# Optimization experiments

Measured on AMD Instinct MI355X. Metric: run time of the kernel, lower is better.

## Reference

```python
import jax, jax.numpy as jnp
import numpy as np

STRIDE = 1
PADDING = 1


def _ternarize(w):
    # threshold = 0.75 * mean(|w|); alpha = mean(|w| over |w| > threshold)
    abs_w = jnp.abs(w)
    threshold = 0.75 * jnp.mean(abs_w)
    mask = abs_w > threshold
    cnt = jnp.sum(mask)
    alpha = jnp.where(cnt > 0, jnp.sum(jnp.where(mask, abs_w, 0.0)) / jnp.maximum(cnt, 1), 1.0)
    tern = jnp.where(w > threshold, alpha, jnp.where(w < -threshold, -alpha, 0.0))
    # straight-through estimator: forward uses tern, grad flows to w as identity
    return w + jax.lax.stop_gradient(tern - w)


def setup_inputs() -> dict:
    key = jax.random.key(0)
    k_x, k_w = jax.random.split(key)
    x = jax.random.normal(k_x, (32, 256, 56, 56), dtype=jnp.float32)
    weight = jax.random.normal(k_w, (256, 256, 3, 3), dtype=jnp.float32)
    return {"x": x, "weight": weight}


def reference(x, weight):
    tw = _ternarize(weight)
    # NCHW input, OIHW kernel
    return jax.lax.conv_general_dilated(
        x, tw,
        window_strides=(STRIDE, STRIDE),
        padding=[(PADDING, PADDING), (PADDING, PADDING)],
        dimension_numbers=("NCHW", "OIHW", "NCHW"),
    )
```

## Files before the change

### kernel.cpp

```cpp
#include <hip/hip_runtime.h>
#include <hip/hip_bf16.h>

typedef short short8 __attribute__((ext_vector_type(8)));
typedef float f32x4 __attribute__((ext_vector_type(4)));

constexpr int N_  = 32;
constexpr int C_  = 256;
constexpr int K_  = 256;
constexpr int H_  = 56;
constexpr int W_  = 56;
constexpr int HW_ = H_ * W_;
constexpr int NW_ = K_ * C_ * 9;

constexpr int TH   = 4;
constexpr int NB   = 14;
constexpr int HR   = 6, HC = 58;
constexpr int NH   = HR * HC;
constexpr int BROW = 80;
constexpr int BSZ  = NH * BROW;
constexpr int NPAIR2 = 8 * NH;
constexpr int SITER  = 6;
constexpr int ASTEP  = 16384;

constexpr int NQB   = 1152;
constexpr int WS_P1 = 4;
constexpr int WS_P2 = 300;
constexpr int WS_P3 = 1500;
constexpr size_t WS_WQ = 16384;
constexpr size_t WS_NEEDED = WS_WQ + (size_t)NW_ * 2;

__device__ __forceinline__ unsigned f2bf(float f) {
    unsigned u = __builtin_bit_cast(unsigned, f);
    return (u + 0x7FFFu + ((u >> 16) & 1u)) >> 16;
}

__global__ void k_abs_partial(const float* __restrict__ w, float* __restrict__ ws) {
    __shared__ float sm[4];
    float s = 0.f;
    for (int i = blockIdx.x * 256 + threadIdx.x; i < NW_; i += 256 * 256)
        s += fabsf(w[i]);
    #pragma unroll
    for (int o = 32; o > 0; o >>= 1) s += __shfl_down(s, o, 64);
    const int wid = threadIdx.x >> 6, lane = threadIdx.x & 63;
    if (lane == 0) sm[wid] = s;
    __syncthreads();
    if (threadIdx.x == 0) {
        float r = 0.f;
        for (int i = 0; i < 4; ++i) r += sm[i];
        ws[WS_P1 + blockIdx.x] = r;
    }
}

__device__ __forceinline__ float reduce256_all(const float* __restrict__ p, float* sm) {
    float v = threadIdx.x < 256 ? p[threadIdx.x] : 0.f;
    #pragma unroll
    for (int o = 32; o > 0; o >>= 1) v += __shfl_down(v, o, 64);
    const int wid = threadIdx.x >> 6, lane = threadIdx.x & 63;
    __syncthreads();
    if (lane == 0) sm[wid] = v;
    __syncthreads();
    float total = 0.f;
    #pragma unroll
    for (int i = 0; i < 8; ++i) total += sm[i];
    return total;
}

__global__ __launch_bounds__(512) void k_quant(const float* __restrict__ w,
                                               float* __restrict__ ws,
                                               unsigned short* __restrict__ wq) {
    __shared__ float sm[8];
    const float total = reduce256_all(ws + WS_P1, sm);
    const float thr = 0.75f * total / (float)NW_;
    const int i = blockIdx.x * 512 + threadIdx.x;
    const float v = w[i];
    const unsigned short q = v > thr ? (unsigned short)0x3F80
                                     : (v < -thr ? (unsigned short)0xBF80 : (unsigned short)0);
    const int k   = i / 2304;
    const int rem = i - k * 2304;
    const int c   = rem / 9;
    const int rs  = rem - c * 9;
    const int chi = c >> 5, c5 = c & 31;
    wq[(size_t)(chi * 9 + rs) * 8192 + (k << 5) + c5] = q;
    const float a = fabsf(v);
    float s = a > thr ? a : 0.f;
    float cn = a > thr ? 1.f : 0.f;
    #pragma unroll
    for (int o = 32; o > 0; o >>= 1) { s += __shfl_down(s, o, 64); cn += __shfl_down(cn, o, 64); }
    __shared__ float sm2[16];
    const int wid = threadIdx.x >> 6, lane = threadIdx.x & 63;
    __syncthreads();
    if (lane == 0) { sm2[wid] = s; sm2[8 + wid] = cn; }
    __syncthreads();
    if (threadIdx.x == 0) {
        float S = 0.f, C2 = 0.f;
        for (int j = 0; j < 8; ++j) { S += sm2[j]; C2 += sm2[8 + j]; }
        ws[WS_P2 + blockIdx.x] = S;
        ws[WS_P3 + blockIdx.x] = C2;
    }
}

__global__ void k_fb_total(float* __restrict__ ws) {
    __shared__ float sm[4];
    float v = ws[WS_P1 + threadIdx.x];
    #pragma unroll
    for (int o = 32; o > 0; o >>= 1) v += __shfl_down(v, o, 64);
    const int wid = threadIdx.x >> 6, lane = threadIdx.x & 63;
    if (lane == 0) sm[wid] = v;
    __syncthreads();
    if (threadIdx.x == 0) {
        float r = 0.f;
        for (int i = 0; i < 4; ++i) r += sm[i];
        ws[0] = r;
    }
}

__global__ void k_fb_masked(const float* __restrict__ w, float* __restrict__ ws) {
    const float thr = 0.75f * ws[0] / (float)NW_;
    float s = 0.f, c = 0.f;
    for (int i = blockIdx.x * 256 + threadIdx.x; i < NW_; i += 256 * 256) {
        float a = fabsf(w[i]);
        if (a > thr) { s += a; c += 1.f; }
    }
    #pragma unroll
    for (int o = 32; o > 0; o >>= 1) { s += __shfl_down(s, o, 64); c += __shfl_down(c, o, 64); }
    __shared__ float sm[8];
    const int wid = threadIdx.x >> 6, lane = threadIdx.x & 63;
    if (lane == 0) { sm[wid] = s; sm[4 + wid] = c; }
    __syncthreads();
    if (threadIdx.x == 0) {
        float S = 0.f, C2 = 0.f;
        for (int i = 0; i < 4; ++i) { S += sm[i]; C2 += sm[i + 4]; }
        ws[WS_P2 + blockIdx.x] = S;
        ws[WS_P3 + blockIdx.x] = C2;
    }
}

__global__ void k_final_masked(float* __restrict__ ws) {
    __shared__ float sm[8];
    float s = ws[WS_P2 + threadIdx.x];
    float c = ws[WS_P3 + threadIdx.x];
    #pragma unroll
    for (int o = 32; o > 0; o >>= 1) { s += __shfl_down(s, o, 64); c += __shfl_down(c, o, 64); }
    const int wid = threadIdx.x >> 6, lane = threadIdx.x & 63;
    if (lane == 0) { sm[wid] = s; sm[4 + wid] = c; }
    __syncthreads();
    if (threadIdx.x == 0) {
        float S = 0.f, C2 = 0.f;
        for (int i = 0; i < 4; ++i) { S += sm[i]; C2 += sm[i + 4]; }
        ws[1] = S; ws[2] = C2;
    }
}

constexpr int RSO_[9] = {
    (0*HC+0)*BROW, (0*HC+1)*BROW, (0*HC+2)*BROW,
    (1*HC+0)*BROW, (1*HC+1)*BROW, (1*HC+2)*BROW,
    (2*HC+0)*BROW, (2*HC+1)*BROW, (2*HC+2)*BROW };

struct ConvState {
    const float* xn;
    const char*  wqc;
    char*        ldsp;
    size_t       aoff;
    int          h0, tid;
    int          bB[7];
};

__device__ __forceinline__ void load_a(short8 (&d)[4], const ConvState& st, int step) {
    const char* ap = st.wqc + (size_t)step * ASTEP + st.aoff;
    d[0] = *(const short8*)(ap);
    d[1] = *(const short8*)(ap + 1024);
    d[2] = *(const short8*)(ap + 2048);
    d[3] = *(const short8*)(ap + 3072);
}

__device__ __forceinline__ void issue_b(const ConvState& st, int c0,
                                        float (&bs)[SITER][4], unsigned& bmask) {
    bmask = 0;
    #pragma unroll
    for (int it = 0; it < SITER; ++it) {
        const int u  = it * 512 + st.tid;
        const bool vu = u < NPAIR2;
        const int uu = vu ? u : 0;
        const int c4 = uu / NH, hidx = uu - c4 * NH;
        const int hy = hidx / HC, hx = hidx - hy * HC;
        const int h  = st.h0 - 1 + hy, w = hx - 1;
        const bool ok = vu && (unsigned)h < (unsigned)H_ && (unsigned)w < (unsigned)W_;
        const int off = ok ? ((c0 + 4 * c4) * HW_ + h * W_ + w) : 0;
        const float* p = st.xn + off;
        bs[it][0] = p[0];
        bs[it][1] = p[HW_];
        bs[it][2] = p[2 * HW_];
        bs[it][3] = p[3 * HW_];
        bmask |= (ok ? 1u : 0u) << it;
    }
}

__device__ __forceinline__ void write_b(const ConvState& st, int base,
                                        const float (&bs)[SITER][4], unsigned bmask) {
    #pragma unroll
    for (int it = 0; it < SITER; ++it) {
        const int u = it * 512 + st.tid;
        if (u < NPAIR2) {
            const int c4 = u / NH, hidx = u - c4 * NH;
            const bool ok = (bmask >> it) & 1u;
            const float f0 = ok ? bs[it][0] : 0.f;
            const float f1 = ok ? bs[it][1] : 0.f;
            const float f2 = ok ? bs[it][2] : 0.f;
            const float f3 = ok ? bs[it][3] : 0.f;
            uint2 v;
            v.x = f2bf(f0) | (f2bf(f1) << 16);
            v.y = f2bf(f2) | (f2bf(f3) << 16);
            *(uint2*)(st.ldsp + base + hidx * BROW + c4 * 8) = v;
        }
    }
}

template <int PAR, bool LASTCH>
__device__ __forceinline__ void do_chunk(int chi, const ConvState& st,
                                         short8 (&afr)[2][4], f32x4 (&acc)[4][7],
                                         float (&bs)[SITER][4], unsigned& bmask) {
    const int rdbase = PAR * BSZ;
    #pragma unroll
    for (int rs = 0; rs < 9; ++rs) {
        const int cur = (PAR + rs) & 1, nxt = cur ^ 1;
        const int step = chi * 9 + rs;
        if (!(LASTCH && rs == 8))
            load_a(afr[nxt], st, step + 1);

        short8 bfr[7];
        #pragma unroll
        for (int nf = 0; nf < 7; ++nf)
            bfr[nf] = *(const short8*)(st.ldsp + rdbase + st.bB[nf] + RSO_[rs]);

        __builtin_amdgcn_s_setprio(1);
        #pragma unroll
        for (int nf = 0; nf < 7; ++nf)
            #pragma unroll
            for (int mf = 0; mf < 4; ++mf)
                acc[mf][nf] = __builtin_amdgcn_mfma_f32_16x16x32_bf16(
                    afr[cur][mf], bfr[nf], acc[mf][nf], 0, 0, 0);
        __builtin_amdgcn_s_setprio(0);

        if (rs == 6 && !LASTCH)
            issue_b(st, (chi + 1) * 32, bs, bmask);
        if (rs == 8 && !LASTCH) {
            write_b(st, (PAR ^ 1) * BSZ, bs, bmask);
            asm volatile("s_waitcnt lgkmcnt(0)" ::: "memory");
            __builtin_amdgcn_s_barrier();
        }
    }
}

__global__ __launch_bounds__(512, 2) void conv_mfma(const float* __restrict__ x,
                                                    const unsigned short* __restrict__ wq,
                                                    const float* __restrict__ wsc,
                                                    float* __restrict__ out) {
    __shared__ char lds[2 * BSZ];
    const int tid = threadIdx.x, lane = tid & 63, wid = tid >> 6;
    const int wm = wid & 3, wn = wid >> 2, lr = lane & 15, lg = lane >> 4;
    const int band = blockIdx.x, n = blockIdx.y;

    ConvState st;
    st.xn   = x + (size_t)n * C_ * HW_;
    st.wqc  = (const char*)wq;
    st.ldsp = lds;
    st.aoff = (size_t)(wm * 64 + lr) * 64 + lg * 16;
    st.h0   = band * TH;
    st.tid  = tid;
    #pragma unroll
    for (int nf = 0; nf < 7; ++nf) {
        const int pos = wn * 112 + nf * 16 + lr;
        const int y = pos / 56, xx = pos - y * 56;
        st.bB[nf] = (y * HC + xx) * BROW + lg * 16;
    }

    f32x4 acc[4][7] = {};
    short8 afr[2][4];
    float bs[SITER][4];
    unsigned bmask;

    issue_b(st, 0, bs, bmask);
    load_a(afr[0], st, 0);
    write_b(st, 0, bs, bmask);
    asm volatile("s_waitcnt lgkmcnt(0)" ::: "memory");
    __builtin_amdgcn_s_barrier();

    for (int cc = 0; cc < 3; ++cc) {
        do_chunk<0, false>(2 * cc,     st, afr, acc, bs, bmask);
        do_chunk<1, false>(2 * cc + 1, st, afr, acc, bs, bmask);
    }
    do_chunk<0, false>(6, st, afr, acc, bs, bmask);
    do_chunk<1, true >(7, st, afr, acc, bs, bmask);

    __syncthreads();
    float* sred = (float*)lds;
    float s2 = wsc[WS_P2 + tid] + wsc[WS_P2 + 512 + tid];
    float s3 = wsc[WS_P3 + tid] + wsc[WS_P3 + 512 + tid];
    if (tid < NQB - 1024) {
        s2 += wsc[WS_P2 + 1024 + tid];
        s3 += wsc[WS_P3 + 1024 + tid];
    }
    #pragma unroll
    for (int o = 32; o > 0; o >>= 1) { s2 += __shfl_down(s2, o, 64); s3 += __shfl_down(s3, o, 64); }
    if (lane == 0) { sred[wid] = s2; sred[8 + wid] = s3; }
    __syncthreads();
    float msum = 0.f, mcnt = 0.f;
    #pragma unroll
    for (int i = 0; i < 8; ++i) { msum += sred[i]; mcnt += sred[8 + i]; }
    const float alpha = mcnt > 0.f ? msum / fmaxf(mcnt, 1.f) : 1.0f;

    #pragma unroll
    for (int mf = 0; mf < 4; ++mf) {
        const int k = wm * 64 + mf * 16 + lg * 4;
        #pragma unroll
        for (int nf = 0; nf < 7; ++nf) {
            const int pos = wn * 112 + nf * 16 + lr;
            const int y = pos / 56, xx = pos - y * 56;
            float* po = out + ((size_t)n * K_ + k) * HW_ + (st.h0 + y) * W_ + xx;
            #pragma unroll
            for (int j = 0; j < 4; ++j)
                po[(size_t)j * HW_] = alpha * acc[mf][nf][j];
        }
    }
}

constexpr int W4_ = W_ / 4;
constexpr int SP_ = H_ * W4_;
__global__ __launch_bounds__(256) void conv_tern_otf(const float* __restrict__ x,
                                                     const float* __restrict__ wt,
                                                     const float* __restrict__ wsc,
                                                     float* __restrict__ out) {
    const int kg = blockIdx.x, n = blockIdx.y, k0 = kg * 4;
    const float thr = 0.75f * wsc[0] / (float)NW_;
    const float cnt = wsc[2];
    const float alpha = cnt > 0.f ? wsc[1] / fmaxf(cnt, 1.f) : 1.0f;
    for (int j = 0; j < 4; ++j) {
        const int sp = (int)threadIdx.x + j * 256;
        if (sp >= SP_) break;
        const int h = sp / W4_, w0 = (sp % W4_) * 4;
        float acc[4][4];
        #pragma unroll
        for (int kt = 0; kt < 4; ++kt)
            #pragma unroll
            for (int jj = 0; jj < 4; ++jj) acc[kt][jj] = 0.f;
        for (int c = 0; c < C_; ++c) {
            const float* xp = x + (((size_t)n * C_ + c) * H_) * W_;
            float xr[3][6];
            #pragma unroll
            for (int r = 0; r < 3; ++r) {
                const int hh = h + r - 1;
                const float* rowp = xp + hh * W_;
                if ((unsigned)hh < (unsigned)H_) {
                    const float4 mid = *(const float4*)(rowp + w0);
                    xr[r][1] = mid.x; xr[r][2] = mid.y; xr[r][3] = mid.z; xr[r][4] = mid.w;
                    xr[r][0] = (w0 > 0)      ? rowp[w0 - 1] : 0.f;
                    xr[r][5] = (w0 + 4 < W_) ? rowp[w0 + 4] : 0.f;
                } else {
                    #pragma unroll
                    for (int q = 0; q < 6; ++q) xr[r][q] = 0.f;
                }
            }
            #pragma unroll
            for (int kt = 0; kt < 4; ++kt) {
                const float* wp = wt + ((size_t)(k0 + kt) * C_ + c) * 9;
                #pragma unroll
                for (int r = 0; r < 3; ++r)
                    #pragma unroll
                    for (int s = 0; s < 3; ++s) {
                        float wv = wp[r * 3 + s];
                        wv = wv > thr ? alpha : (wv < -thr ? -alpha : 0.f);
                        #pragma unroll
                        for (int jj = 0; jj < 4; ++jj)
                            acc[kt][jj] = fmaf(wv, xr[r][jj + s], acc[kt][jj]);
                    }
            }
        }
        #pragma unroll
        for (int kt = 0; kt < 4; ++kt) {
            float4 o;
            o.x = acc[kt][0]; o.y = acc[kt][1]; o.z = acc[kt][2]; o.w = acc[kt][3];
            *(float4*)(out + ((((size_t)n * K_ + (k0 + kt)) * H_ + h) * W_ + w0)) = o;
        }
    }
}

extern "C" void kernel_launch(void* const* d_in, const int* in_sizes, int n_in,
                              void* d_out, int out_size, void* d_ws, size_t ws_size,
                              hipStream_t stream) {
    const float* x = (const float*)d_in[0];
    const float* w = (const float*)d_in[1];
    float* out = (float*)d_out;
    float* ws  = (float*)d_ws;
    unsigned short* wq = (unsigned short*)((char*)d_ws + WS_WQ);

    k_abs_partial<<<256, 256, 0, stream>>>(w, ws);

    if (ws_size >= WS_NEEDED) {
        k_quant<<<NQB, 512, 0, stream>>>(w, ws, wq);
        dim3 grid(NB, N_);
        conv_mfma<<<grid, 512, 0, stream>>>(x, wq, ws, out);
    } else {
        k_fb_total<<<1, 256, 0, stream>>>(ws);
        k_fb_masked<<<256, 256, 0, stream>>>(w, ws);
        k_final_masked<<<1, 256, 0, stream>>>(ws);
        dim3 grid(64, N_);
        conv_tern_otf<<<grid, 256, 0, stream>>>(x, w, ws, out);
    }
}
```

Before: 128.3 us.

## Split output channels across two 256-thread blocks and stage B loads in two phases

The conv kernel now uses 256-thread blocks with four waves, and each block covers half of the 256 output channels, selected by a new kz index. The grid doubles along x so that twice as many blocks exist. Loading the input tile into LDS is split into two staged issue/write phases (6 then 5 iterations) spread across the filter taps, which bounds register use. Each block still stages the full input halo, so global and LDS input traffic and the bf16 conversion work are duplicated per output-channel half, in exchange for smaller blocks and more of them per CU.

```diff
diff --git a/kernel.cpp b/kernel.cpp
--- a/kernel.cpp
+++ b/kernel.cpp
@@ -19,7 +19,6 @@
 constexpr int BROW = 80;
 constexpr int BSZ  = NH * BROW;
 constexpr int NPAIR2 = 8 * NH;
-constexpr int SITER  = 6;
 constexpr int ASTEP  = 16384;
 
 constexpr int NQB   = 1152;
@@ -173,12 +172,13 @@
     d[3] = *(const short8*)(ap + 3072);
 }
 
-__device__ __forceinline__ void issue_b(const ConvState& st, int c0,
-                                        float (&bs)[SITER][4], unsigned& bmask) {
+template <int IT0, int NIT>
+__device__ __forceinline__ void issue_bx(const ConvState& st, int c0,
+                                         float (&bs)[6][4], unsigned& bmask) {
     bmask = 0;
     #pragma unroll
-    for (int it = 0; it < SITER; ++it) {
-        const int u  = it * 512 + st.tid;
+    for (int j = 0; j < NIT; ++j) {
+        const int u  = (IT0 + j) * 256 + st.tid;
         const bool vu = u < NPAIR2;
         const int uu = vu ? u : 0;
         const int c4 = uu / NH, hidx = uu - c4 * NH;
@@ -187,26 +187,27 @@
         const bool ok = vu && (unsigned)h < (unsigned)H_ && (unsigned)w < (unsigned)W_;
         const int off = ok ? ((c0 + 4 * c4) * HW_ + h * W_ + w) : 0;
         const float* p = st.xn + off;
-        bs[it][0] = p[0];
-        bs[it][1] = p[HW_];
-        bs[it][2] = p[2 * HW_];
-        bs[it][3] = p[3 * HW_];
-        bmask |= (ok ? 1u : 0u) << it;
-    }
-}
-
-__device__ __forceinline__ void write_b(const ConvState& st, int base,
-                                        const float (&bs)[SITER][4], unsigned bmask) {
-    #pragma unroll
-    for (int it = 0; it < SITER; ++it) {
-        const int u = it * 512 + st.tid;
+        bs[j][0] = p[0];
+        bs[j][1] = p[HW_];
+        bs[j][2] = p[2 * HW_];
+        bs[j][3] = p[3 * HW_];
+        bmask |= (ok ? 1u : 0u) << j;
+    }
+}
+
+template <int IT0, int NIT>
+__device__ __forceinline__ void write_bx(const ConvState& st, int base,
+                                         const float (&bs)[6][4], unsigned bmask) {
+    #pragma unroll
+    for (int j = 0; j < NIT; ++j) {
+        const int u = (IT0 + j) * 256 + st.tid;
         if (u < NPAIR2) {
             const int c4 = u / NH, hidx = u - c4 * NH;
-            const bool ok = (bmask >> it) & 1u;
-            const float f0 = ok ? bs[it][0] : 0.f;
-            const float f1 = ok ? bs[it][1] : 0.f;
-            const float f2 = ok ? bs[it][2] : 0.f;
-            const float f3 = ok ? bs[it][3] : 0.f;
+            const bool ok = (bmask >> j) & 1u;
+            const float f0 = ok ? bs[j][0] : 0.f;
+            const float f1 = ok ? bs[j][1] : 0.f;
+            const float f2 = ok ? bs[j][2] : 0.f;
+            const float f3 = ok ? bs[j][3] : 0.f;
             uint2 v;
             v.x = f2bf(f0) | (f2bf(f1) << 16);
             v.y = f2bf(f2) | (f2bf(f3) << 16);
@@ -218,8 +219,9 @@
 template <int PAR, bool LASTCH>
 __device__ __forceinline__ void do_chunk(int chi, const ConvState& st,
                                          short8 (&afr)[2][4], f32x4 (&acc)[4][7],
-                                         float (&bs)[SITER][4], unsigned& bmask) {
+                                         float (&bs)[6][4], unsigned& bmask) {
     const int rdbase = PAR * BSZ;
+    const int wrbase = (PAR ^ 1) * BSZ;
     #pragma unroll
     for (int rs = 0; rs < 9; ++rs) {
         const int cur = (PAR + rs) & 1, nxt = cur ^ 1;
@@ -241,30 +243,35 @@
                     afr[cur][mf], bfr[nf], acc[mf][nf], 0, 0, 0);
         __builtin_amdgcn_s_setprio(0);
 
-        if (rs == 6 && !LASTCH)
-            issue_b(st, (chi + 1) * 32, bs, bmask);
-        if (rs == 8 && !LASTCH) {
-            write_b(st, (PAR ^ 1) * BSZ, bs, bmask);
-            asm volatile("s_waitcnt lgkmcnt(0)" ::: "memory");
-            __builtin_amdgcn_s_barrier();
+        if (!LASTCH) {
+            if (rs == 4) {
+                issue_bx<0, 6>(st, (chi + 1) * 32, bs, bmask);
+            } else if (rs == 6) {
+                write_bx<0, 6>(st, wrbase, bs, bmask);
+                issue_bx<6, 5>(st, (chi + 1) * 32, bs, bmask);
+            } else if (rs == 8) {
+                write_bx<6, 5>(st, wrbase, bs, bmask);
+                asm volatile("s_waitcnt lgkmcnt(0)" ::: "memory");
+                __builtin_amdgcn_s_barrier();
+            }
         }
     }
 }
 
-__global__ __launch_bounds__(512, 2) void conv_mfma(const float* __restrict__ x,
+__global__ __launch_bounds__(256, 2) void conv_mfma(const float* __restrict__ x,
                                                     const unsigned short* __restrict__ wq,
                                                     const float* __restrict__ wsc,
                                                     float* __restrict__ out) {
     __shared__ char lds[2 * BSZ];
     const int tid = threadIdx.x, lane = tid & 63, wid = tid >> 6;
-    const int wm = wid & 3, wn = wid >> 2, lr = lane & 15, lg = lane >> 4;
-    const int band = blockIdx.x, n = blockIdx.y;
-
+    const int wm = wid & 1, wn = wid >> 1, lr = lane & 15, lg = lane >> 4;
+    const int bx = blockIdx.x, n = blockIdx.y;
+    const int band = bx >> 1, kz = bx & 1;
     ConvState st;
     st.xn   = x + (size_t)n * C_ * HW_;
     st.wqc  = (const char*)wq;
     st.ldsp = lds;
-    st.aoff = (size_t)(wm * 64 + lr) * 64 + lg * 16;
+    st.aoff = (size_t)(kz * 128 + wm * 64 + lr) * 64 + lg * 16;
     st.h0   = band * TH;
     st.tid  = tid;
     #pragma unroll
@@ -276,12 +283,14 @@
 
     f32x4 acc[4][7] = {};
     short8 afr[2][4];
-    float bs[SITER][4];
+    float bs[6][4];
     unsigned bmask;
 
-    issue_b(st, 0, bs, bmask);
     load_a(afr[0], st, 0);
-    write_b(st, 0, bs, bmask);
+    issue_bx<0, 6>(st, 0, bs, bmask);
+    write_bx<0, 6>(st, 0, bs, bmask);
+    issue_bx<6, 5>(st, 0, bs, bmask);
+    write_bx<6, 5>(st, 0, bs, bmask);
     asm volatile("s_waitcnt lgkmcnt(0)" ::: "memory");
     __builtin_amdgcn_s_barrier();
 
@@ -294,24 +303,26 @@
 
     __syncthreads();
     float* sred = (float*)lds;
-    float s2 = wsc[WS_P2 + tid] + wsc[WS_P2 + 512 + tid];
-    float s3 = wsc[WS_P3 + tid] + wsc[WS_P3 + 512 + tid];
+    float s2 = wsc[WS_P2 + tid] + wsc[WS_P2 + 256 + tid]
+             + wsc[WS_P2 + 512 + tid] + wsc[WS_P2 + 768 + tid];
+    float s3 = wsc[WS_P3 + tid] + wsc[WS_P3 + 256 + tid]
+             + wsc[WS_P3 + 512 + tid] + wsc[WS_P3 + 768 + tid];
     if (tid < NQB - 1024) {
         s2 += wsc[WS_P2 + 1024 + tid];
         s3 += wsc[WS_P3 + 1024 + tid];
     }
     #pragma unroll
     for (int o = 32; o > 0; o >>= 1) { s2 += __shfl_down(s2, o, 64); s3 += __shfl_down(s3, o, 64); }
-    if (lane == 0) { sred[wid] = s2; sred[8 + wid] = s3; }
+    if (lane == 0) { sred[wid] = s2; sred[4 + wid] = s3; }
     __syncthreads();
     float msum = 0.f, mcnt = 0.f;
     #pragma unroll
-    for (int i = 0; i < 8; ++i) { msum += sred[i]; mcnt += sred[8 + i]; }
+    for (int i = 0; i < 4; ++i) { msum += sred[i]; mcnt += sred[4 + i]; }
     const float alpha = mcnt > 0.f ? msum / fmaxf(mcnt, 1.f) : 1.0f;
 
     #pragma unroll
     for (int mf = 0; mf < 4; ++mf) {
-        const int k = wm * 64 + mf * 16 + lg * 4;
+        const int k = kz * 128 + wm * 64 + mf * 16 + lg * 4;
         #pragma unroll
         for (int nf = 0; nf < 7; ++nf) {
             const int pos = wn * 112 + nf * 16 + lr;
@@ -397,8 +408,8 @@
 
     if (ws_size >= WS_NEEDED) {
         k_quant<<<NQB, 512, 0, stream>>>(w, ws, wq);
-        dim3 grid(NB, N_);
-        conv_mfma<<<grid, 512, 0, stream>>>(x, wq, ws, out);
+        dim3 grid(2 * NB, N_);
+        conv_mfma<<<grid, 256, 0, stream>>>(x, wq, ws, out);
     } else {
         k_fb_total<<<1, 256, 0, stream>>>(ws);
         k_fb_masked<<<256, 256, 0, stream>>>(w, ws);
```

Result: slower. 164.7 us (+28.4%).
